# Kernel optimization log

Hardware: AMD Instinct MI355X
Metric: run time of the kernel (lower is better)

Reference implementation:

```python
import jax, jax.numpy as jnp
import numpy as np

V = 8192        # num_embeddings == n_nodes
E = 262144      # n_edges (avg degree 32)
N = 262144      # lookup batch
D = 128         # out_channels
LAMDA = 0.8
EPS = 1e-12


def setup_inputs() -> dict:
    key = jax.random.key(0)
    k0, k1, k2, k3, k4 = jax.random.split(key, 5)
    x = jax.random.randint(k0, (N,), 0, V)
    edge_index = jax.random.randint(k1, (2, E), 0, V)
    edge_weight = jax.random.uniform(k2, (E,), dtype=jnp.float32)
    embedding = jax.random.normal(k3, (V, V), dtype=jnp.float32) * 0.02
    W = jax.random.normal(k4, (V, D), dtype=jnp.float32) * (1.0 / np.sqrt(V))
    b = jnp.zeros((D,), dtype=jnp.float32)
    return {"x": x, "edge_index": edge_index, "edge_weight": edge_weight,
            "embedding": embedding, "W": W, "b": b}


def reference(x, edge_index, edge_weight, embedding, W, b):
    # Embedding_sim: linear transform then sparse adjacency propagation
    H = embedding @ W + b                       # [V, D]
    src, dst = edge_index[0], edge_index[1]
    msg = H[src] * edge_weight[:, None]         # gather + weight, [E, D]
    P = jax.ops.segment_sum(msg, dst, num_segments=V)  # spmm(A, H), [V, D]
    emb = LAMDA * P + (1.0 - LAMDA) * H         # [V, D]
    # dropout is identity in eval mode
    out = emb[x]                                # embedding lookup, [N, D]
    norm = jnp.linalg.norm(out, axis=-1, keepdims=True)
    return out / jnp.maximum(norm, EPS)         # F.normalize (L2, dim=1)
```

## Files before the change

kernel.cpp:

```cpp
#include <hip/hip_runtime.h>
#include <hip/hip_bf16.h>

#define V     8192
#define E_N   262144
#define NN    262144
#define D     128
#define KDIM  8192

typedef __attribute__((ext_vector_type(8))) short b16x8;
typedef __attribute__((ext_vector_type(4))) float f32x4;

static __device__ __forceinline__ unsigned short f2bf(float f) {
    union { float f; unsigned int u; } v; v.f = f;
    unsigned int r = v.u + 0x7FFFu + ((v.u >> 16) & 1u);
    return (unsigned short)(r >> 16);
}

static __device__ __forceinline__ unsigned int cvtpk(float lo, float hi) {
    unsigned int r;
    asm("v_cvt_pk_bf16_f32 %0, %1, %2" : "=v"(r) : "v"(lo), "v"(hi));
    return r;
}

__global__ void k_pack(const float* __restrict__ W, unsigned short* __restrict__ Wp,
                       int* __restrict__ cursor) {
    __shared__ float tile[32][129];
    int kb = blockIdx.x;
    int t  = threadIdx.x;
    if (kb < 32) cursor[kb * 256 + t] = 0;
    #pragma unroll
    for (int i = 0; i < 16; i++) {
        int lin = i * 256 + t;
        int kk = lin >> 7, c = lin & 127;
        tile[kk][c] = W[(size_t)(kb * 32 + kk) * D + c];
    }
    __syncthreads();
    unsigned short* outp = Wp + (size_t)kb * 4096;
    #pragma unroll
    for (int i = 0; i < 16; i++) {
        int o = i * 256 + t;
        int c = o >> 5, kk = o & 31;
        outp[o] = f2bf(tile[kk][c]);
    }
}

__global__ void k_hist(const int* __restrict__ dst, int* __restrict__ hist) {
    int e = blockIdx.x * 256 + threadIdx.x;
    if (e < E_N) atomicAdd(&hist[dst[e]], 1);
}

__global__ void k_scan(const int* __restrict__ hist, int* __restrict__ offsets,
                       int* __restrict__ cursor) {
    __shared__ int part[1024];
    int t = threadIdx.x;
    int base = t * 8;
    int loc[8]; int s = 0;
    for (int i = 0; i < 8; i++) { loc[i] = s; s += hist[base + i]; }
    part[t] = s;
    __syncthreads();
    for (int st = 1; st < 1024; st <<= 1) {
        int v = (t >= st) ? part[t - st] : 0;
        __syncthreads();
        part[t] += v;
        __syncthreads();
    }
    int ex = (t == 0) ? 0 : part[t - 1];
    for (int i = 0; i < 8; i++) {
        int o = ex + loc[i];
        offsets[base + i] = o;
        cursor[base + i] = o;
    }
    if (t == 1023) offsets[8192] = ex + s;
}

__global__ void k_scatter(const int* __restrict__ srcI, const int* __restrict__ dstI,
                          const float* __restrict__ w, int* __restrict__ cursor,
                          int* __restrict__ src_s, float* __restrict__ w_s) {
    int e = blockIdx.x * 256 + threadIdx.x;
    if (e < E_N) {
        int dnode = dstI[e];
        int pos = atomicAdd(&cursor[dnode], 1);
        src_s[pos] = srcI[e];
        w_s[pos]  = w[e];
    }
}

__global__ void __launch_bounds__(256, 2) k_gemm(const float* __restrict__ A,
                                                 const unsigned short* __restrict__ Wp,
                                                 float* __restrict__ Hp) {
    const int rb   = blockIdx.x >> 2;
    const int ks   = blockIdx.x & 3;
    const int tid  = threadIdx.x;
    const int w    = tid >> 6;
    const int lane = tid & 63;
    const int r16  = lane & 15;
    const int kg   = lane >> 4;

    const float* aP = A + (size_t)(rb * 64 + w * 16 + r16) * KDIM + ks * 2048 + kg * 8;
    const unsigned short* bP = Wp + (size_t)(ks * 64) * 4096 + r16 * 32 + kg * 8;

    f32x4 acc[8];
    f32x4 zero = {0.f, 0.f, 0.f, 0.f};
    #pragma unroll
    for (int t = 0; t < 8; t++) acc[t] = zero;

#define LDA(s0, s1, p)                                                  \
    do { const float* ap_ = aP + (size_t)(p) * 32;                      \
         s0 = *(const f32x4*)ap_; s1 = *(const f32x4*)(ap_ + 4); } while (0)
#define LDB(bb, p)                                                      \
    do { const b16x8* bp_ = (const b16x8*)(bP + (size_t)(p) * 4096);    \
         _Pragma("unroll")                                              \
         for (int t = 0; t < 8; t++) bb[t] = bp_[t * 64]; } while (0)
#define COMP(s0, s1, bb)                                                \
    do { union { b16x8 v; unsigned int u[4]; } af_;                     \
         af_.u[0] = cvtpk(s0[0], s0[1]);                                \
         af_.u[1] = cvtpk(s0[2], s0[3]);                                \
         af_.u[2] = cvtpk(s1[0], s1[1]);                                \
         af_.u[3] = cvtpk(s1[2], s1[3]);                                \
         _Pragma("unroll")                                              \
         for (int t = 0; t < 8; t++)                                    \
             acc[t] = __builtin_amdgcn_mfma_f32_16x16x32_bf16(af_.v, bb[t], acc[t], 0, 0, 0); \
    } while (0)
#define CL(p) ((p) < 64 ? (p) : 63)

    f32x4 a00, a01, a10, a11, a20, a21, a30, a31;
    b16x8 b0[8], b1[8];

    LDA(a00, a01, 0);
    LDA(a10, a11, 1);
    LDB(b0, 0);
    LDA(a20, a21, 2);
    LDB(b1, 1);
    LDA(a30, a31, 3);

    for (int p = 0; p < 64; p += 4) {
        COMP(a00, a01, b0); LDB(b0, CL(p + 2)); LDA(a00, a01, CL(p + 4));
        COMP(a10, a11, b1); LDB(b1, CL(p + 3)); LDA(a10, a11, CL(p + 5));
        COMP(a20, a21, b0); LDB(b0, CL(p + 4)); LDA(a20, a21, CL(p + 6));
        COMP(a30, a31, b1); LDB(b1, CL(p + 5)); LDA(a30, a31, CL(p + 7));
    }
#undef LDA
#undef LDB
#undef COMP
#undef CL

    float* hp = Hp + ((size_t)ks * V + (size_t)(rb * 64 + w * 16 + kg * 4)) * D + r16;
    #pragma unroll
    for (int t = 0; t < 8; t++)
        #pragma unroll
        for (int j = 0; j < 4; j++)
            hp[(size_t)j * D + t * 16] = acc[t][j];
}

__global__ void k_comb(const float* __restrict__ Hp, const float* __restrict__ b,
                       float* __restrict__ H) {
    int i = blockIdx.x * 256 + threadIdx.x;
    f32x4 bb = *(const f32x4*)(b + (i & 31) * 4);
    const f32x4* hp = (const f32x4*)Hp;
    const size_t q = (size_t)V * D / 4;
    f32x4 s = bb + hp[i] + hp[i + q] + hp[i + 2 * q] + hp[i + 3 * q];
    ((f32x4*)H)[i] = s;
}

__global__ void k_emb(const float* __restrict__ H, const int* __restrict__ offsets,
                      const int* __restrict__ src_s, const float* __restrict__ w_s,
                      float* __restrict__ embn) {
    __shared__ float red[128];
    int v = blockIdx.x;
    int d = threadIdx.x;
    int s0 = offsets[v], s1 = offsets[v + 1];
    float acc = 0.f;
    for (int i = s0; i < s1; i++) {
        int s = src_s[i];
        float w = w_s[i];
        acc = fmaf(w, H[(size_t)s * D + d], acc);
    }
    float e = 0.8f * acc + 0.2f * H[(size_t)v * D + d];
    red[d] = e * e;
    __syncthreads();
    for (int st = 64; st > 0; st >>= 1) {
        if (d < st) red[d] += red[d + st];
        __syncthreads();
    }
    float norm = sqrtf(red[0]);
    float scale = 1.f / fmaxf(norm, 1e-12f);
    embn[(size_t)v * D + d] = e * scale;
}

__global__ void k_out(const int* __restrict__ x, const float* __restrict__ embn,
                      float* __restrict__ out) {
    int t = blockIdx.x * 256 + threadIdx.x;
    int n = t >> 5, c = t & 31;
    int xv = x[n];
    ((f32x4*)out)[t] = ((const f32x4*)embn)[xv * 32 + c];
}

extern "C" void kernel_launch(void* const* d_in, const int* in_sizes, int n_in,
                              void* d_out, int out_size, void* d_ws, size_t ws_size,
                              hipStream_t stream) {
    const int*   x      = (const int*)d_in[0];
    const int*   eSrc   = (const int*)d_in[1];
    const int*   eDst   = ((const int*)d_in[1]) + E_N;
    const float* eW     = (const float*)d_in[2];
    const float* A      = (const float*)d_in[3];
    const float* W      = (const float*)d_in[4];
    const float* b      = (const float*)d_in[5];
    float* out = (float*)d_out;

    char* ws = (char*)d_ws;
    unsigned short* Wp  = (unsigned short*)(ws);
    float* H            = (float*)(ws + (2u << 20));
    float* embn         = (float*)(ws + (6u << 20));
    float* Hp           = (float*)(ws + (10u << 20));
    int* offsets        = (int*)(ws + (26u << 20));
    int* cursor         = (int*)(ws + (26u << 20) + 40960);
    int* src_s          = (int*)(ws + (26u << 20) + 131072);
    float* w_s          = (float*)(ws + (26u << 20) + 131072 + (1u << 20));

    k_pack   <<<256, 256, 0, stream>>>(W, Wp, cursor);
    k_hist   <<<E_N / 256, 256, 0, stream>>>(eDst, cursor);
    k_scan   <<<1, 1024, 0, stream>>>(cursor, offsets, cursor);
    k_scatter<<<E_N / 256, 256, 0, stream>>>(eSrc, eDst, eW, cursor, src_s, w_s);
    k_gemm   <<<512, 256, 0, stream>>>(A, Wp, Hp);
    k_comb   <<<(V * D / 4) / 256, 256, 0, stream>>>(Hp, b, H);
    k_emb    <<<V, D, 0, stream>>>(H, offsets, src_s, w_s, embn);
    k_out    <<<(NN * 32) / 256, 256, 0, stream>>>(x, embn, out);
}
```

Baseline: 219.6 us.

## Stage GEMM tiles through swizzled LDS via direct global-to-LDS loads, split-K 8

Rewrites the dense GEMM so each block loads A and packed-W tiles into double-buffered, XOR-swizzled shared memory with global_load_lds, and waves share B fragments across a 2x2 wave layout. Split-K goes from 4 to 8 with 1024 blocks and 4 blocks per CU, and the combine kernel sums 8 partials. The aim is to cut redundant per-wave global B loads and raise occupancy for the 256 MB fp32 A stream. The cost is extra barriers, a larger partial buffer and more combine traffic, with the workspace layout shifted to fit.

```diff
diff --git a/kernel.cpp b/kernel.cpp
--- a/kernel.cpp
+++ b/kernel.cpp
@@ -6,6 +6,7 @@
 #define NN    262144
 #define D     128
 #define KDIM  8192
+#define SPLITK 8
 
 typedef __attribute__((ext_vector_type(8))) short b16x8;
 typedef __attribute__((ext_vector_type(4))) float f32x4;
@@ -85,80 +86,120 @@
     }
 }
 
-__global__ void __launch_bounds__(256, 2) k_gemm(const float* __restrict__ A,
+__global__ void __launch_bounds__(256, 4) k_gemm(const float* __restrict__ A,
                                                  const unsigned short* __restrict__ Wp,
                                                  float* __restrict__ Hp) {
-    const int rb   = blockIdx.x >> 2;
-    const int ks   = blockIdx.x & 3;
-    const int tid  = threadIdx.x;
-    const int w    = tid >> 6;
-    const int lane = tid & 63;
-    const int r16  = lane & 15;
-    const int kg   = lane >> 4;
-
-    const float* aP = A + (size_t)(rb * 64 + w * 16 + r16) * KDIM + ks * 2048 + kg * 8;
-    const unsigned short* bP = Wp + (size_t)(ks * 64) * 4096 + r16 * 32 + kg * 8;
-
-    f32x4 acc[8];
+    __shared__ float          As[2][64][32];
+    __shared__ unsigned short Bs[2][128][32];
+
+    const int rb  = blockIdx.x >> 3;
+    const int ks  = blockIdx.x & 7;
+    const int tid = threadIdx.x;
+    const int w   = tid >> 6;
+    const int l   = tid & 63;
+    const int r16 = l & 15;
+    const int kg  = l >> 4;
+    const int wm  = w & 1, wn = w >> 1;
+
+    const int aSwz = ((l & 7) ^ ((l >> 3) & 7)) * 4;
+    const float* aSrc0 = A + (size_t)(rb * 64 + w * 16 + (l >> 3)) * KDIM
+                           + ks * 1024 + aSwz;
+    const float* aSrc1 = aSrc0 + (size_t)8 * KDIM;
+    const int bSwz = ((l & 3) ^ ((l >> 3) & 3)) * 8;
+    const unsigned short* bSrc0 = Wp + (size_t)(ks * 32) * 4096 + (w * 32 + (l >> 2)) * 32 + bSwz;
+    const unsigned short* bSrc1 = bSrc0 + 16 * 32;
+
+    f32x4 acc[2][4];
     f32x4 zero = {0.f, 0.f, 0.f, 0.f};
     #pragma unroll
-    for (int t = 0; t < 8; t++) acc[t] = zero;
-
-#define LDA(s0, s1, p)                                                  \
-    do { const float* ap_ = aP + (size_t)(p) * 32;                      \
-         s0 = *(const f32x4*)ap_; s1 = *(const f32x4*)(ap_ + 4); } while (0)
-#define LDB(bb, p)                                                      \
-    do { const b16x8* bp_ = (const b16x8*)(bP + (size_t)(p) * 4096);    \
-         _Pragma("unroll")                                              \
-         for (int t = 0; t < 8; t++) bb[t] = bp_[t * 64]; } while (0)
-#define COMP(s0, s1, bb)                                                \
-    do { union { b16x8 v; unsigned int u[4]; } af_;                     \
-         af_.u[0] = cvtpk(s0[0], s0[1]);                                \
-         af_.u[1] = cvtpk(s0[2], s0[3]);                                \
-         af_.u[2] = cvtpk(s1[0], s1[1]);                                \
-         af_.u[3] = cvtpk(s1[2], s1[3]);                                \
-         _Pragma("unroll")                                              \
-         for (int t = 0; t < 8; t++)                                    \
-             acc[t] = __builtin_amdgcn_mfma_f32_16x16x32_bf16(af_.v, bb[t], acc[t], 0, 0, 0); \
+    for (int m = 0; m < 2; m++)
+        #pragma unroll
+        for (int n = 0; n < 4; n++) acc[m][n] = zero;
+
+#define STAGE(nb, t)                                                                     \
+    do {                                                                                 \
+        __builtin_amdgcn_global_load_lds(                                                \
+            (const __attribute__((address_space(1))) void*)(aSrc0 + (size_t)(t) * 32),   \
+            (__attribute__((address_space(3))) void*)&As[nb][w * 16][0], 16, 0, 0);      \
+        __builtin_amdgcn_global_load_lds(                                                \
+            (const __attribute__((address_space(1))) void*)(aSrc1 + (size_t)(t) * 32),   \
+            (__attribute__((address_space(3))) void*)&As[nb][w * 16 + 8][0], 16, 0, 0);  \
+        __builtin_amdgcn_global_load_lds(                                                \
+            (const __attribute__((address_space(1))) void*)(bSrc0 + (size_t)(t) * 4096), \
+            (__attribute__((address_space(3))) void*)&Bs[nb][w * 32][0], 16, 0, 0);      \
+        __builtin_amdgcn_global_load_lds(                                                \
+            (const __attribute__((address_space(1))) void*)(bSrc1 + (size_t)(t) * 4096), \
+            (__attribute__((address_space(3))) void*)&Bs[nb][w * 32 + 16][0], 16, 0, 0); \
     } while (0)
-#define CL(p) ((p) < 64 ? (p) : 63)
-
-    f32x4 a00, a01, a10, a11, a20, a21, a30, a31;
-    b16x8 b0[8], b1[8];
-
-    LDA(a00, a01, 0);
-    LDA(a10, a11, 1);
-    LDB(b0, 0);
-    LDA(a20, a21, 2);
-    LDB(b1, 1);
-    LDA(a30, a31, 3);
-
-    for (int p = 0; p < 64; p += 4) {
-        COMP(a00, a01, b0); LDB(b0, CL(p + 2)); LDA(a00, a01, CL(p + 4));
-        COMP(a10, a11, b1); LDB(b1, CL(p + 3)); LDA(a10, a11, CL(p + 5));
-        COMP(a20, a21, b0); LDB(b0, CL(p + 4)); LDA(a20, a21, CL(p + 6));
-        COMP(a30, a31, b1); LDB(b1, CL(p + 5)); LDA(a30, a31, CL(p + 7));
-    }
-#undef LDA
-#undef LDB
-#undef COMP
-#undef CL
-
-    float* hp = Hp + ((size_t)ks * V + (size_t)(rb * 64 + w * 16 + kg * 4)) * D + r16;
-    #pragma unroll
-    for (int t = 0; t < 8; t++)
+
+#define COMPUTE(nb)                                                                      \
+    do {                                                                                 \
+        const float* abase = &As[nb][0][0];                                              \
+        const unsigned short* bbase = &Bs[nb][0][0];                                     \
+        const int s0 = (2 * kg) ^ (r16 & 7);                                             \
+        const int s1 = (2 * kg + 1) ^ (r16 & 7);                                         \
+        const int sb = kg ^ ((r16 >> 1) & 3);                                            \
+        b16x8 bf[4];                                                                     \
+        _Pragma("unroll")                                                                \
+        for (int n = 0; n < 4; n++) {                                                    \
+            int col = wn * 64 + n * 16 + r16;                                            \
+            bf[n] = *(const b16x8*)(bbase + col * 32 + sb * 8);                          \
+        }                                                                                \
+        _Pragma("unroll")                                                                \
+        for (int m = 0; m < 2; m++) {                                                    \
+            int row = wm * 32 + m * 16 + r16;                                            \
+            f32x4 a0 = *(const f32x4*)(abase + row * 32 + s0 * 4);                       \
+            f32x4 a1 = *(const f32x4*)(abase + row * 32 + s1 * 4);                       \
+            union { b16x8 v; unsigned int u[4]; } af;                                    \
+            af.u[0] = cvtpk(a0[0], a0[1]);                                               \
+            af.u[1] = cvtpk(a0[2], a0[3]);                                               \
+            af.u[2] = cvtpk(a1[0], a1[1]);                                               \
+            af.u[3] = cvtpk(a1[2], a1[3]);                                               \
+            _Pragma("unroll")                                                            \
+            for (int n = 0; n < 4; n++)                                                  \
+                acc[m][n] = __builtin_amdgcn_mfma_f32_16x16x32_bf16(af.v, bf[n],         \
+                                                                    acc[m][n], 0, 0, 0); \
+        }                                                                                \
+    } while (0)
+
+    STAGE(0, 0);
+    asm volatile("s_waitcnt vmcnt(0)" ::: "memory");
+    __builtin_amdgcn_s_barrier();
+
+    int nb = 0;
+    for (int t = 0; t < 31; ++t) {
+        STAGE(nb ^ 1, t + 1);
+        COMPUTE(nb);
+        asm volatile("s_waitcnt vmcnt(0)" ::: "memory");
+        __builtin_amdgcn_s_barrier();
+        nb ^= 1;
+    }
+    COMPUTE(nb);
+#undef STAGE
+#undef COMPUTE
+
+    #pragma unroll
+    for (int m = 0; m < 2; m++) {
+        int row0 = rb * 64 + wm * 32 + m * 16 + kg * 4;
         #pragma unroll
-        for (int j = 0; j < 4; j++)
-            hp[(size_t)j * D + t * 16] = acc[t][j];
+        for (int n = 0; n < 4; n++) {
+            int col = wn * 64 + n * 16 + r16;
+            float* hp = Hp + ((size_t)ks * V + row0) * D + col;
+            #pragma unroll
+            for (int j = 0; j < 4; j++)
+                hp[(size_t)j * D] = acc[m][n][j];
+        }
+    }
 }
 
 __global__ void k_comb(const float* __restrict__ Hp, const float* __restrict__ b,
                        float* __restrict__ H) {
     int i = blockIdx.x * 256 + threadIdx.x;
-    f32x4 bb = *(const f32x4*)(b + (i & 31) * 4);
+    f32x4 s = *(const f32x4*)(b + (i & 31) * 4);
     const f32x4* hp = (const f32x4*)Hp;
     const size_t q = (size_t)V * D / 4;
-    f32x4 s = bb + hp[i] + hp[i + q] + hp[i + 2 * q] + hp[i + 3 * q];
+    #pragma unroll
+    for (int k = 0; k < SPLITK; k++) s += hp[i + k * q];
     ((f32x4*)H)[i] = s;
 }
 
@@ -212,16 +253,16 @@
     float* H            = (float*)(ws + (2u << 20));
     float* embn         = (float*)(ws + (6u << 20));
     float* Hp           = (float*)(ws + (10u << 20));
-    int* offsets        = (int*)(ws + (26u << 20));
-    int* cursor         = (int*)(ws + (26u << 20) + 40960);
-    int* src_s          = (int*)(ws + (26u << 20) + 131072);
-    float* w_s          = (float*)(ws + (26u << 20) + 131072 + (1u << 20));
+    int* offsets        = (int*)(ws + (42u << 20));
+    int* cursor         = (int*)(ws + (42u << 20) + 40960);
+    int* src_s          = (int*)(ws + (42u << 20) + 131072);
+    float* w_s          = (float*)(ws + (42u << 20) + 131072 + (1u << 20));
 
     k_pack   <<<256, 256, 0, stream>>>(W, Wp, cursor);
     k_hist   <<<E_N / 256, 256, 0, stream>>>(eDst, cursor);
     k_scan   <<<1, 1024, 0, stream>>>(cursor, offsets, cursor);
     k_scatter<<<E_N / 256, 256, 0, stream>>>(eSrc, eDst, eW, cursor, src_s, w_s);
-    k_gemm   <<<512, 256, 0, stream>>>(A, Wp, Hp);
+    k_gemm   <<<1024, 256, 0, stream>>>(A, Wp, Hp);
     k_comb   <<<(V * D / 4) / 256, 256, 0, stream>>>(Hp, b, H);
     k_emb    <<<V, D, 0, stream>>>(H, offsets, src_s, w_s, embn);
     k_out    <<<(NN * 32) / 256, 256, 0, stream>>>(x, embn, out);
```

After: 208.1 us. 5.2% less time.

## Stage GEMM A tiles through LDS via direct global-to-LDS swizzled loads

Applied to the files above, without the earlier changes.

The split-K GEMM no longer loads fp32 A fragments straight into registers with a register-level prefetch pipeline. Each wave now copies a 16x256 A slab into LDS with global_load_lds, using an XOR swizzle to avoid bank conflicts, and reads bf16 fragments back from LDS. The intent is fully coalesced row loads for the large A matrix. In exchange, the kernel waits on all outstanding loads at every step, so A fetches no longer overlap compute across steps, and it uses 64KB of LDS per block. The bias-combine loop is also rewritten as a loop over SPLITK.

```diff
diff --git a/kernel.cpp b/kernel.cpp
--- a/kernel.cpp
+++ b/kernel.cpp
@@ -6,6 +6,7 @@
 #define NN    262144
 #define D     128
 #define KDIM  8192
+#define SPLITK 4
 
 typedef __attribute__((ext_vector_type(8))) short b16x8;
 typedef __attribute__((ext_vector_type(4))) float f32x4;
@@ -88,61 +89,77 @@
 __global__ void __launch_bounds__(256, 2) k_gemm(const float* __restrict__ A,
                                                  const unsigned short* __restrict__ Wp,
                                                  float* __restrict__ Hp) {
-    const int rb   = blockIdx.x >> 2;
-    const int ks   = blockIdx.x & 3;
-    const int tid  = threadIdx.x;
-    const int w    = tid >> 6;
-    const int lane = tid & 63;
-    const int r16  = lane & 15;
-    const int kg   = lane >> 4;
-
-    const float* aP = A + (size_t)(rb * 64 + w * 16 + r16) * KDIM + ks * 2048 + kg * 8;
-    const unsigned short* bP = Wp + (size_t)(ks * 64) * 4096 + r16 * 32 + kg * 8;
+    __shared__ float As[64][256];
+
+    const int rb  = blockIdx.x >> 2;
+    const int ks  = blockIdx.x & 3;
+    const int tid = threadIdx.x;
+    const int w   = tid >> 6;
+    const int l   = tid & 63;
+    const int r16 = l & 15;
+    const int kg  = l >> 4;
+
+    const float* aRow0 = A + (size_t)(rb * 64 + w * 16) * KDIM + ks * 2048;
+    const unsigned short* bKS = Wp + (size_t)(ks * 64) * 4096 + r16 * 32 + kg * 8;
 
     f32x4 acc[8];
     f32x4 zero = {0.f, 0.f, 0.f, 0.f};
     #pragma unroll
     for (int t = 0; t < 8; t++) acc[t] = zero;
 
-#define LDA(s0, s1, p)                                                  \
-    do { const float* ap_ = aP + (size_t)(p) * 32;                      \
-         s0 = *(const f32x4*)ap_; s1 = *(const f32x4*)(ap_ + 4); } while (0)
-#define LDB(bb, p)                                                      \
-    do { const b16x8* bp_ = (const b16x8*)(bP + (size_t)(p) * 4096);    \
-         _Pragma("unroll")                                              \
-         for (int t = 0; t < 8; t++) bb[t] = bp_[t * 64]; } while (0)
-#define COMP(s0, s1, bb)                                                \
-    do { union { b16x8 v; unsigned int u[4]; } af_;                     \
-         af_.u[0] = cvtpk(s0[0], s0[1]);                                \
-         af_.u[1] = cvtpk(s0[2], s0[3]);                                \
-         af_.u[2] = cvtpk(s1[0], s1[1]);                                \
-         af_.u[3] = cvtpk(s1[2], s1[3]);                                \
-         _Pragma("unroll")                                              \
-         for (int t = 0; t < 8; t++)                                    \
-             acc[t] = __builtin_amdgcn_mfma_f32_16x16x32_bf16(af_.v, bb[t], acc[t], 0, 0, 0); \
+#define LDB(arr, stepBase, sub)                                                     \
+    do { const unsigned short* bp_ = bKS + (size_t)((stepBase) + (sub)) * 4096;     \
+         _Pragma("unroll")                                                          \
+         for (int t = 0; t < 8; ++t) arr[t] = *(const b16x8*)(bp_ + t * 512);       \
     } while (0)
-#define CL(p) ((p) < 64 ? (p) : 63)
-
-    f32x4 a00, a01, a10, a11, a20, a21, a30, a31;
-    b16x8 b0[8], b1[8];
-
-    LDA(a00, a01, 0);
-    LDA(a10, a11, 1);
-    LDB(b0, 0);
-    LDA(a20, a21, 2);
-    LDB(b1, 1);
-    LDA(a30, a31, 3);
-
-    for (int p = 0; p < 64; p += 4) {
-        COMP(a00, a01, b0); LDB(b0, CL(p + 2)); LDA(a00, a01, CL(p + 4));
-        COMP(a10, a11, b1); LDB(b1, CL(p + 3)); LDA(a10, a11, CL(p + 5));
-        COMP(a20, a21, b0); LDB(b0, CL(p + 4)); LDA(a20, a21, CL(p + 6));
-        COMP(a30, a31, b1); LDB(b1, CL(p + 5)); LDA(a30, a31, CL(p + 7));
-    }
-#undef LDA
+
+#define AFRAG(af, sub)                                                              \
+    do { int g0 = (sub) * 8 + kg * 2;                                               \
+         f32x4 x0 = *(const f32x4*)&As[w * 16 + r16][((g0)     ^ (r16 & 7)) << 2];  \
+         f32x4 x1 = *(const f32x4*)&As[w * 16 + r16][((g0 + 1) ^ (r16 & 7)) << 2];  \
+         af.u[0] = cvtpk(x0[0], x0[1]);  af.u[1] = cvtpk(x0[2], x0[3]);             \
+         af.u[2] = cvtpk(x1[0], x1[1]);  af.u[3] = cvtpk(x1[2], x1[3]); } while (0)
+
+#define MF(af, arr)                                                                 \
+    do { _Pragma("unroll")                                                          \
+         for (int t = 0; t < 8; ++t)                                                \
+             acc[t] = __builtin_amdgcn_mfma_f32_16x16x32_bf16(af.v, arr[t],         \
+                                                              acc[t], 0, 0, 0); } while (0)
+
+#define SUB(s, CUR, NXT, stepBase)                                                  \
+    do { if ((s) < 7) LDB(NXT, stepBase, (s) + 1);                                  \
+         union { b16x8 v; unsigned int u[4]; } af_;                                 \
+         AFRAG(af_, s);                                                             \
+         MF(af_, CUR); } while (0)
+
+    for (int step = 0; step < 8; ++step) {
+        const float* aStep = aRow0 + step * 256;
+        #pragma unroll
+        for (int r = 0; r < 16; ++r) {
+            __builtin_amdgcn_global_load_lds(
+                (const __attribute__((address_space(1))) void*)
+                    (aStep + (size_t)r * KDIM + ((l ^ (r & 7)) << 2)),
+                (__attribute__((address_space(3))) void*)&As[w * 16 + r][0], 16, 0, 0);
+        }
+
+        b16x8 b0[8], b1[8];
+        LDB(b0, step * 8, 0);
+
+        asm volatile("s_waitcnt vmcnt(0)" ::: "memory");
+
+        SUB(0, b0, b1, step * 8);
+        SUB(1, b1, b0, step * 8);
+        SUB(2, b0, b1, step * 8);
+        SUB(3, b1, b0, step * 8);
+        SUB(4, b0, b1, step * 8);
+        SUB(5, b1, b0, step * 8);
+        SUB(6, b0, b1, step * 8);
+        SUB(7, b1, b0, step * 8);
+    }
 #undef LDB
-#undef COMP
-#undef CL
+#undef AFRAG
+#undef MF
+#undef SUB
 
     float* hp = Hp + ((size_t)ks * V + (size_t)(rb * 64 + w * 16 + kg * 4)) * D + r16;
     #pragma unroll
@@ -155,10 +172,11 @@
 __global__ void k_comb(const float* __restrict__ Hp, const float* __restrict__ b,
                        float* __restrict__ H) {
     int i = blockIdx.x * 256 + threadIdx.x;
-    f32x4 bb = *(const f32x4*)(b + (i & 31) * 4);
+    f32x4 s = *(const f32x4*)(b + (i & 31) * 4);
     const f32x4* hp = (const f32x4*)Hp;
     const size_t q = (size_t)V * D / 4;
-    f32x4 s = bb + hp[i] + hp[i + q] + hp[i + 2 * q] + hp[i + 3 * q];
+    #pragma unroll
+    for (int k = 0; k < SPLITK; k++) s += hp[i + k * q];
     ((f32x4*)H)[i] = s;
 }
 
```

Measured after the change: 213.3 us. -2.9%, faster.
